# Kernel tuning notes

Measured on AMD Instinct MI355X. Metric: run time of the kernel, lower is better.

## Reference

```python
import jax, jax.numpy as jnp
from jax import lax
import numpy as np

N = 262144    # input_size (mesh nodes)
B = 16        # batch of snapshots
LAT = 16      # dims_latent
HID = 512     # intermediate fc width
NFC = 16      # num_final_channels
START = 4097  # inv_conv_start
SPLIT = NFC * START
SFC = 2       # number of space-filling curves
K, S, P = 32, 4, 16             # kernel/stride/padding (dimension==2)
OPS = (1, 1, 0)                 # output_paddings of decoder convT chain
CH = ((16, 8), (8, 4), (4, 1))  # (in,out) channels per decoder convT layer


def conv_t(x, w, b, op):
    # torch ConvTranspose1d: w [Cin,Cout,K], stride=S, padding=P, output_padding=op
    # equivalent to lhs-dilated cross-correlation with flipped, transposed kernel
    rhs = jnp.flip(w, -1).transpose(1, 0, 2)  # [Cout,Cin,K]
    y = lax.conv_general_dilated(x, rhs, (1,), [(K - 1 - P, K - 1 - P + op)],
                                 lhs_dilation=(S,),
                                 dimension_numbers=('NCH', 'OIH', 'NCH'))
    return y + b[None, :, None]


def setup_inputs() -> dict:
    key = jax.random.key(0)
    ks = jax.random.split(key, 32)
    inp = {}
    inp['x'] = jax.random.normal(ks[0], (B, LAT), jnp.float32)
    inp['fc1_w'] = jax.random.normal(ks[1], (LAT, HID), jnp.float32) * 0.1
    inp['fc1_b'] = jnp.zeros((HID,), jnp.float32)
    inp['fc2_w'] = jax.random.normal(ks[2], (HID, SFC * SPLIT), jnp.float32) * 0.02
    inp['fc2_b'] = jnp.zeros((SFC * SPLIT,), jnp.float32)
    idx = 3
    for i in range(SFC):
        for j, (ci, co) in enumerate(CH):
            inp[f'ct{i}{j}_w'] = jax.random.normal(ks[idx], (ci, co, K), jnp.float32) * 0.05
            inp[f'ct{i}{j}_b'] = jnp.zeros((co,), jnp.float32)
            idx += 1
        # NearestNeighbouring(size=N, initial_weight=1/3, num_neigh=3)
        inp[f'sp{i}_w'] = jnp.full((N, 3), 1.0 / 3.0, jnp.float32)
        inp[f'sp{i}_b'] = jnp.zeros((N,), jnp.float32)
        oi = jax.random.permutation(ks[idx], N).astype(jnp.int32)
        idx += 1
        inp[f'ord{i}'] = oi
        inp[f'minus{i}'] = jnp.concatenate([oi[:1], oi[:-1]])  # find_minus_neigh
        inp[f'plus{i}'] = jnp.concatenate([oi[1:], oi[-1:]])   # find_plus_neigh
    # final_sp: NearestNeighbouring(size=N, initial_weight=1/sfc_nums, num_neigh=sfc_nums)
    inp['fsp_w'] = jnp.full((N, SFC), 1.0 / SFC, jnp.float32)
    inp['fsp_b'] = jnp.zeros((N,), jnp.float32)
    return inp


def reference(x, fc1_w, fc1_b, fc2_w, fc2_b,
              ct00_w, ct00_b, ct01_w, ct01_b, ct02_w, ct02_b,
              ct10_w, ct10_b, ct11_w, ct11_b, ct12_w, ct12_b,
              sp0_w, sp0_b, sp1_w, sp1_b, fsp_w, fsp_b,
              ord0, minus0, plus0, ord1, minus1, plus1):
    act = jnp.tanh  # unstructured default activation
    h = act(x @ fc1_w + fc1_b)
    h = act(h @ fc2_w + fc2_b)          # [B, SFC*SPLIT]
    h = h.reshape(-1, SPLIT, SFC)
    cts = (((ct00_w, ct00_b), (ct01_w, ct01_b), (ct02_w, ct02_b)),
           ((ct10_w, ct10_b), (ct11_w, ct11_b), (ct12_w, ct12_b)))
    sps = ((sp0_w, sp0_b), (sp1_w, sp1_b))
    ords = ((minus0, ord0, plus0), (minus1, ord1, plus1))
    zs = []
    for i in range(SFC):
        b = h[..., i].reshape(-1, NFC, START)   # [B,16,4097]
        for j in range(len(CH)):
            w, bb = cts[i][j]
            b = act(conv_t(b, w, bb, OPS[j]))
        b = b.reshape(-1, N)                    # [B, N]
        m, o, p = ords[i]
        # SFC gather of (minus, self, plus) neighbors -> [B, N, 3]
        tt = jnp.stack([b[:, m], b[:, o], b[:, p]], axis=-1)
        w, bb = sps[i]
        zs.append(act(jnp.sum(tt * w, -1) + bb))
    # combine the SFC branches with the final learned weighted sum
    z = act(jnp.sum(jnp.stack(zs, -1) * fsp_w, -1) + fsp_b)  # [B, N]
    return z
```

## Files before the change

### kernel.cpp

```cpp
#include <hip/hip_runtime.h>
#include <hip/hip_bf16.h>

#define BATCH 16
#define LAT 16
#define HID 512
#define NFC 16
#define START_ 4097
#define NSFC 2
#define NMESH 262144
#define JTOT 131104
#define HB_BR_STRIDE 1048832

#define L1 16385
#define L1S 16388
#define L2 65537
#define L2S 65540
#define L3 262144

#define Y1_SZ (BATCH*8*L1S)
#define Y2_SZ (BATCH*4*L2S)
#define Y3_SZ (BATCH*L3)

__global__ __launch_bounds__(256) void k_fc1(const float* __restrict__ x,
                                             const float* __restrict__ w,
                                             const float* __restrict__ bias,
                                             float* __restrict__ h1) {
    int j = blockIdx.x * 256 + threadIdx.x;
    float acc[BATCH];
    float bv = bias[j];
#pragma unroll
    for (int b = 0; b < BATCH; ++b) acc[b] = bv;
#pragma unroll
    for (int k = 0; k < LAT; ++k) {
        float wv = w[k * HID + j];
#pragma unroll
        for (int b = 0; b < BATCH; ++b)
            acc[b] = fmaf(x[b * LAT + k], wv, acc[b]);
    }
#pragma unroll
    for (int b = 0; b < BATCH; ++b) h1[b * HID + j] = tanhf(acc[b]);
}

__global__ __launch_bounds__(256) void k_fc2(const float* __restrict__ h1,
                                             const float* __restrict__ w,
                                             const float* __restrict__ bias,
                                             float* __restrict__ hb) {
    int j = blockIdx.x * 256 + threadIdx.x;
    if (j >= JTOT) return;
    float acc[BATCH];
    float bv = bias[j];
#pragma unroll
    for (int b = 0; b < BATCH; ++b) acc[b] = bv;
#pragma unroll 8
    for (int k = 0; k < HID; ++k) {
        float wv = w[(size_t)k * JTOT + j];
#pragma unroll
        for (int b = 0; b < BATCH; ++b)
            acc[b] = fmaf(h1[b * HID + k], wv, acc[b]);
    }
    int i = j & 1;
    int s = j >> 1;
    int c = s / START_;
    int t = s - c * START_;
    float* hp = hb + (size_t)i * HB_BR_STRIDE + c * START_ + t;
#pragma unroll
    for (int b = 0; b < BATCH; ++b)
        hp[(size_t)b * (NFC * START_)] = tanhf(acc[b]);
}

template <int CIN, int COUT, int WCO, int WT>
__global__ __launch_bounds__(256) void k_conv(const float* __restrict__ xb,
                                              float* __restrict__ yb,
                                              const float* __restrict__ w0g,
                                              const float* __restrict__ w1g,
                                              const float* __restrict__ b0g,
                                              const float* __restrict__ b1g,
                                              int LIN, int LINS, int LOUT, int LOUTS,
                                              int xbs, int ybs) {
    constexpr int SROW = WT * 256 + 12;
    constexpr int SROW4 = SROW / 4;
    __shared__ __align__(16) float sx[CIN * SROW];

    const int br = blockIdx.z;
    const float* x = xb + (size_t)br * xbs;
    float* y = yb + (size_t)br * ybs;
    const float* wg = br ? w1g : w0g;
    const float* bg = br ? b1g : b0g;
    const int b = blockIdx.y;
    const int t0 = blockIdx.x * (WT * 1024);
    const int q0 = (t0 + 16) >> 2;

    for (int idx = threadIdx.x; idx < CIN * SROW; idx += 256) {
        int ci = idx / SROW;
        int sr = idx - ci * SROW;
        int s = q0 - 8 + sr;
        sx[idx] = (s >= 0 && s < LIN) ? x[(size_t)(b * CIN + ci) * LINS + s] : 0.f;
    }
    __syncthreads();

    const int wv = __builtin_amdgcn_readfirstlane((int)(threadIdx.x >> 6));
    const int lane = threadIdx.x & 63;
    constexpr int WAVES_CO = 4 / WT;
    const int wt = wv / WAVES_CO;
    const int co0 = (wv % WAVES_CO) * WCO;

    float acc[WCO][16];
#pragma unroll
    for (int cw = 0; cw < WCO; ++cw) {
        float bv = bg[co0 + cw];
#pragma unroll
        for (int e = 0; e < 16; ++e) acc[cw][e] = bv;
    }

    const int qrel4 = wt * 64 + lane;
    const float4* sx4 = (const float4*)sx;
#pragma unroll 1
    for (int ci = 0; ci < CIN; ++ci) {
        float4 A = sx4[ci * SROW4 + qrel4];
        float4 Bv = sx4[ci * SROW4 + qrel4 + 1];
        float4 Cv = sx4[ci * SROW4 + qrel4 + 2];
        float xv[12] = {A.x, A.y, A.z, A.w, Bv.x, Bv.y, Bv.z, Bv.w,
                        Cv.x, Cv.y, Cv.z, Cv.w};
        const float* wp = wg + (ci * COUT + co0) * 32;
#pragma unroll
        for (int cw = 0; cw < WCO; ++cw) {
            const float* wpc = wp + cw * 32;
#pragma unroll
            for (int d = 0; d < 8; ++d)
#pragma unroll
                for (int m = 0; m < 4; ++m)
#pragma unroll
                    for (int j = 0; j < 4; ++j)
                        acc[cw][m * 4 + j] =
                            fmaf(xv[m + 8 - d], wpc[4 * d + j], acc[cw][m * 4 + j]);
        }
    }

    const int t_lane = t0 + wt * 1024 + lane * 16;
#pragma unroll
    for (int cw = 0; cw < WCO; ++cw) {
        float* yp = y + (size_t)(b * COUT + co0 + cw) * LOUTS + t_lane;
        if (t_lane + 15 < LOUT) {
#pragma unroll
            for (int c4 = 0; c4 < 4; ++c4) {
                float4 o;
                o.x = tanhf(acc[cw][c4 * 4 + 0]);
                o.y = tanhf(acc[cw][c4 * 4 + 1]);
                o.z = tanhf(acc[cw][c4 * 4 + 2]);
                o.w = tanhf(acc[cw][c4 * 4 + 3]);
                ((float4*)yp)[c4] = o;
            }
        } else {
            for (int e = 0; e < 16; ++e)
                if (t_lane + e < LOUT) yp[e] = tanhf(acc[cw][e]);
        }
    }
}

#define C3_TT 256
#define C3_SW 71

__global__ __launch_bounds__(256) void k_conv3t(const float* __restrict__ y2g,
                                                float* __restrict__ y3t,
                                                const float* __restrict__ w0g,
                                                const float* __restrict__ w1g,
                                                const float* __restrict__ b0g,
                                                const float* __restrict__ b1g,
                                                int xbs, int ybs) {
    __shared__ float sx[BATCH * 4 * C3_SW];

    const int br = blockIdx.z;
    const float* x = y2g + (size_t)br * xbs;
    float* y = y3t + (size_t)br * ybs;
    const float* wg = br ? w1g : w0g;
    const float bv = (br ? b1g : b0g)[0];

    const int t0 = blockIdx.x * C3_TT;
    const int q0 = (t0 >> 2) + 4;
    const int s0 = q0 - 7;

    for (int idx = threadIdx.x; idx < BATCH * 4 * C3_SW; idx += 256) {
        int row = idx / C3_SW;
        int col = idx - row * C3_SW;
        int s = s0 + col;
        sx[idx] = (s >= 0 && s < L2) ? x[(size_t)row * L2S + s] : 0.f;
    }
    __syncthreads();

    const int q = threadIdx.x >> 2;
    const int bg = threadIdx.x & 3;

    float acc[4][4];
#pragma unroll
    for (int r = 0; r < 4; ++r)
#pragma unroll
        for (int bo = 0; bo < 4; ++bo) acc[r][bo] = bv;

#pragma unroll
    for (int ci = 0; ci < 4; ++ci) {
        const float* wp = wg + ci * 32;
#pragma unroll
        for (int bo = 0; bo < 4; ++bo) {
            const float* sp = sx + ((bg * 4 + bo) * 4 + ci) * C3_SW + q;
            float xv[8];
#pragma unroll
            for (int j = 0; j < 8; ++j) xv[j] = sp[j];
#pragma unroll
            for (int d = 0; d < 8; ++d)
#pragma unroll
                for (int r = 0; r < 4; ++r)
                    acc[r][bo] = fmaf(xv[7 - d], wp[4 * d + r], acc[r][bo]);
        }
    }

    const int tbase = t0 + 4 * q;
#pragma unroll
    for (int r = 0; r < 4; ++r) {
        float* yp = y + (size_t)(tbase + r) * BATCH + bg * 4;
        float4 o;
        o.x = tanhf(acc[r][0]);
        o.y = tanhf(acc[r][1]);
        o.z = tanhf(acc[r][2]);
        o.w = tanhf(acc[r][3]);
        *(float4*)yp = o;
    }
}

__global__ __launch_bounds__(256) void k_final(const float* __restrict__ y3t0,
                                               const float* __restrict__ y3t1,
                                               const int* __restrict__ ord0,
                                               const int* __restrict__ ord1,
                                               const float* __restrict__ sw0,
                                               const float* __restrict__ sb0,
                                               const float* __restrict__ sw1,
                                               const float* __restrict__ sb1,
                                               const float* __restrict__ fw,
                                               const float* __restrict__ fb,
                                               float* __restrict__ out) {
    __shared__ int i0[258], i1[258];
    __shared__ float c0[BATCH][264], c1[BATCH][264];
    const int tid = threadIdx.x;
    const int n0 = blockIdx.x * 256;
    const int n = n0 + tid;

    for (int jj = tid; jj < 258; jj += 256) {
        int nn = n0 - 1 + jj;
        nn = nn < 0 ? 0 : (nn > NMESH - 1 ? NMESH - 1 : nn);
        i0[jj] = ord0[nn];
        i1[jj] = ord1[nn];
    }
    __syncthreads();

    for (int kk = tid; kk < 258 * 4; kk += 256) {
        int jj = kk >> 2;
        int v = kk & 3;
        float4 a = *(const float4*)(y3t0 + (size_t)i0[jj] * BATCH + v * 4);
        c0[v * 4 + 0][jj] = a.x;
        c0[v * 4 + 1][jj] = a.y;
        c0[v * 4 + 2][jj] = a.z;
        c0[v * 4 + 3][jj] = a.w;
        float4 bq = *(const float4*)(y3t1 + (size_t)i1[jj] * BATCH + v * 4);
        c1[v * 4 + 0][jj] = bq.x;
        c1[v * 4 + 1][jj] = bq.y;
        c1[v * 4 + 2][jj] = bq.z;
        c1[v * 4 + 3][jj] = bq.w;
    }

    const float w00 = sw0[n * 3], w01 = sw0[n * 3 + 1], w02 = sw0[n * 3 + 2];
    const float w10 = sw1[n * 3], w11 = sw1[n * 3 + 1], w12 = sw1[n * 3 + 2];
    const float s0b = sb0[n], s1b = sb1[n];
    const float f0 = fw[n * 2], f1 = fw[n * 2 + 1], fbv = fb[n];
    __syncthreads();

#pragma unroll
    for (int b = 0; b < BATCH; ++b) {
        float z0 = tanhf(w00 * c0[b][tid] + w01 * c0[b][tid + 1] + w02 * c0[b][tid + 2] + s0b);
        float z1 = tanhf(w10 * c1[b][tid] + w11 * c1[b][tid + 1] + w12 * c1[b][tid + 2] + s1b);
        out[b * NMESH + n] = tanhf(f0 * z0 + f1 * z1 + fbv);
    }
}

extern "C" void kernel_launch(void* const* d_in, const int* in_sizes, int n_in,
                              void* d_out, int out_size, void* d_ws, size_t ws_size,
                              hipStream_t stream) {
    const float* x     = (const float*)d_in[0];
    const float* fc1_w = (const float*)d_in[1];
    const float* fc1_b = (const float*)d_in[2];
    const float* fc2_w = (const float*)d_in[3];
    const float* fc2_b = (const float*)d_in[4];
    const float* ctw[2][3] = {{(const float*)d_in[5], (const float*)d_in[7], (const float*)d_in[9]},
                              {(const float*)d_in[16], (const float*)d_in[18], (const float*)d_in[20]}};
    const float* ctb[2][3] = {{(const float*)d_in[6], (const float*)d_in[8], (const float*)d_in[10]},
                              {(const float*)d_in[17], (const float*)d_in[19], (const float*)d_in[21]}};
    const float* sp0w = (const float*)d_in[11];
    const float* sp0b = (const float*)d_in[12];
    const int*   ord0 = (const int*)d_in[13];
    const float* sp1w = (const float*)d_in[22];
    const float* sp1b = (const float*)d_in[23];
    const int*   ord1 = (const int*)d_in[24];
    const float* fspw = (const float*)d_in[27];
    const float* fspb = (const float*)d_in[28];
    float* out = (float*)d_out;
    float* ws = (float*)d_ws;

    const size_t OFF_H1 = 0;
    const size_t OFF_HB = 8192;
    const size_t OFF_Y1p = OFF_HB + 2ull * HB_BR_STRIDE;
    const size_t OFF_Y2p = OFF_Y1p + 2ull * Y1_SZ;
    const size_t OFF_Y3p = OFF_Y2p + 2ull * Y2_SZ;
    const size_t END_P = OFF_Y3p + 2ull * Y3_SZ;
    const size_t OFF_Y1s = OFF_HB + 2ull * HB_BR_STRIDE;
    const size_t OFF_Y2s = OFF_Y1s + (size_t)Y1_SZ;
    const size_t OFF_Y3s = OFF_Y2s + (size_t)Y2_SZ;

    const bool par = ws_size >= END_P * sizeof(float);

    k_fc1<<<2, 256, 0, stream>>>(x, fc1_w, fc1_b, ws + OFF_H1);
    k_fc2<<<(JTOT + 255) / 256, 256, 0, stream>>>(ws + OFF_H1, fc2_w, fc2_b, ws + OFF_HB);

    float* y3_0;
    float* y3_1;
    if (par) {
        float* hb = ws + OFF_HB;
        float* y1 = ws + OFF_Y1p;
        float* y2 = ws + OFF_Y2p;
        float* y3 = ws + OFF_Y3p;
        k_conv<16, 8, 2, 1><<<dim3(17, BATCH, 2), 256, 0, stream>>>(
            hb, y1, ctw[0][0], ctw[1][0], ctb[0][0], ctb[1][0],
            START_, START_, L1, L1S, HB_BR_STRIDE, Y1_SZ);
        k_conv<8, 4, 1, 1><<<dim3(65, BATCH, 2), 256, 0, stream>>>(
            y1, y2, ctw[0][1], ctw[1][1], ctb[0][1], ctb[1][1],
            L1, L1S, L2, L2S, Y1_SZ, Y2_SZ);
        k_conv3t<<<dim3(L3 / C3_TT, 1, 2), 256, 0, stream>>>(
            y2, y3, ctw[0][2], ctw[1][2], ctb[0][2], ctb[1][2],
            Y2_SZ, Y3_SZ);
        y3_0 = y3;
        y3_1 = y3 + Y3_SZ;
    } else {
        float* y1 = ws + OFF_Y1s;
        float* y2 = ws + OFF_Y2s;
        for (int i = 0; i < 2; ++i) {
            float* hb_i = ws + OFF_HB + (size_t)i * HB_BR_STRIDE;
            float* y3_i = ws + OFF_Y3s + (size_t)i * Y3_SZ;
            k_conv<16, 8, 2, 1><<<dim3(17, BATCH, 1), 256, 0, stream>>>(
                hb_i, y1, ctw[i][0], ctw[i][0], ctb[i][0], ctb[i][0],
                START_, START_, L1, L1S, 0, 0);
            k_conv<8, 4, 1, 1><<<dim3(65, BATCH, 1), 256, 0, stream>>>(
                y1, y2, ctw[i][1], ctw[i][1], ctb[i][1], ctb[i][1],
                L1, L1S, L2, L2S, 0, 0);
            k_conv3t<<<dim3(L3 / C3_TT, 1, 1), 256, 0, stream>>>(
                y2, y3_i, ctw[i][2], ctw[i][2], ctb[i][2], ctb[i][2],
                0, 0);
        }
        y3_0 = ws + OFF_Y3s;
        y3_1 = ws + OFF_Y3s + Y3_SZ;
    }

    k_final<<<NMESH / 256, 256, 0, stream>>>(y3_0, y3_1, ord0, ord1,
                                             sp0w, sp0b, sp1w, sp1b,
                                             fspw, fspb, out);
}
```

Baseline: 579.7 us.

## Fuse second and third transposed convolutions; use fast exp2-based tanh

Merges the conv layer 2 and conv layer 3 kernels into one. Each block computes a halo tile of the intermediate 4-channel output in shared memory, then applies the final conv straight from it, so the y2 buffer is never written to or read from global memory. All tanhf calls are also replaced with an exp2/rcp approximation to cut transcendental cost. The cost is recomputing the halo of the intermediate layer, and tanh accuracy drops, with possible inf handling issues for large inputs.

Result: no change. 588.0 us (+1.4%).

```diff
diff --git a/kernel.cpp b/kernel.cpp
--- a/kernel.cpp
+++ b/kernel.cpp
@@ -14,12 +14,15 @@
 #define L1 16385
 #define L1S 16388
 #define L2 65537
-#define L2S 65540
 #define L3 262144
 
 #define Y1_SZ (BATCH*8*L1S)
-#define Y2_SZ (BATCH*4*L2S)
 #define Y3_SZ (BATCH*L3)
+
+__device__ __forceinline__ float tanh_fast(float x) {
+    float e = __builtin_amdgcn_exp2f(x * 2.8853900817779268f);
+    return 1.0f - 2.0f * __builtin_amdgcn_rcpf(e + 1.0f);
+}
 
 __global__ __launch_bounds__(256) void k_fc1(const float* __restrict__ x,
                                              const float* __restrict__ w,
@@ -38,7 +41,7 @@
             acc[b] = fmaf(x[b * LAT + k], wv, acc[b]);
     }
 #pragma unroll
-    for (int b = 0; b < BATCH; ++b) h1[b * HID + j] = tanhf(acc[b]);
+    for (int b = 0; b < BATCH; ++b) h1[b * HID + j] = tanh_fast(acc[b]);
 }
 
 __global__ __launch_bounds__(256) void k_fc2(const float* __restrict__ h1,
@@ -65,7 +68,7 @@
     float* hp = hb + (size_t)i * HB_BR_STRIDE + c * START_ + t;
 #pragma unroll
     for (int b = 0; b < BATCH; ++b)
-        hp[(size_t)b * (NFC * START_)] = tanhf(acc[b]);
+        hp[(size_t)b * (NFC * START_)] = tanh_fast(acc[b]);
 }
 
 template <int CIN, int COUT, int WCO, int WT>
@@ -144,85 +147,134 @@
 #pragma unroll
             for (int c4 = 0; c4 < 4; ++c4) {
                 float4 o;
-                o.x = tanhf(acc[cw][c4 * 4 + 0]);
-                o.y = tanhf(acc[cw][c4 * 4 + 1]);
-                o.z = tanhf(acc[cw][c4 * 4 + 2]);
-                o.w = tanhf(acc[cw][c4 * 4 + 3]);
+                o.x = tanh_fast(acc[cw][c4 * 4 + 0]);
+                o.y = tanh_fast(acc[cw][c4 * 4 + 1]);
+                o.z = tanh_fast(acc[cw][c4 * 4 + 2]);
+                o.w = tanh_fast(acc[cw][c4 * 4 + 3]);
                 ((float4*)yp)[c4] = o;
             }
         } else {
             for (int e = 0; e < 16; ++e)
-                if (t_lane + e < LOUT) yp[e] = tanhf(acc[cw][e]);
-        }
-    }
-}
-
-#define C3_TT 256
-#define C3_SW 71
-
-__global__ __launch_bounds__(256) void k_conv3t(const float* __restrict__ y2g,
-                                                float* __restrict__ y3t,
-                                                const float* __restrict__ w0g,
-                                                const float* __restrict__ w1g,
-                                                const float* __restrict__ b0g,
-                                                const float* __restrict__ b1g,
-                                                int xbs, int ybs) {
-    __shared__ float sx[BATCH * 4 * C3_SW];
+                if (t_lane + e < LOUT) yp[e] = tanh_fast(acc[cw][e]);
+        }
+    }
+}
+
+#define F_Y1W 25
+#define F_Y2W 73
+
+__global__ __launch_bounds__(256) void k_conv23t(const float* __restrict__ y1g,
+                                                 float* __restrict__ y3t,
+                                                 const float* __restrict__ w20,
+                                                 const float* __restrict__ w21,
+                                                 const float* __restrict__ b20,
+                                                 const float* __restrict__ b21,
+                                                 const float* __restrict__ w30,
+                                                 const float* __restrict__ w31,
+                                                 const float* __restrict__ b30,
+                                                 const float* __restrict__ b31,
+                                                 int xbs, int ybs) {
+    __shared__ float s_y1[BATCH * 8 * F_Y1W];
+    __shared__ float s_y2[BATCH * 4 * F_Y2W];
 
     const int br = blockIdx.z;
-    const float* x = y2g + (size_t)br * xbs;
+    const float* x1 = y1g + (size_t)br * xbs;
     float* y = y3t + (size_t)br * ybs;
-    const float* wg = br ? w1g : w0g;
-    const float bv = (br ? b1g : b0g)[0];
-
-    const int t0 = blockIdx.x * C3_TT;
-    const int q0 = (t0 >> 2) + 4;
-    const int s0 = q0 - 7;
-
-    for (int idx = threadIdx.x; idx < BATCH * 4 * C3_SW; idx += 256) {
-        int row = idx / C3_SW;
-        int col = idx - row * C3_SW;
-        int s = s0 + col;
-        sx[idx] = (s >= 0 && s < L2) ? x[(size_t)row * L2S + s] : 0.f;
+    const float* w2 = br ? w21 : w20;
+    const float b2v_all = 0.f; (void)b2v_all;
+    const float* b2 = br ? b21 : b20;
+    const float* w3 = br ? w31 : w30;
+    const float b3v = (br ? b31 : b30)[0];
+
+    const int bx = blockIdx.x;
+    const int T0 = bx * 256;
+    const int Q1_0 = (T0 >> 4) - 4;
+    const int S2_0 = (T0 >> 2) - 4;
+
+    for (int idx = threadIdx.x; idx < BATCH * 8 * F_Y1W; idx += 256) {
+        int row = idx / F_Y1W;
+        int col = idx - row * F_Y1W;
+        int q1 = Q1_0 + col;
+        s_y1[idx] = (q1 >= 0 && q1 < L1) ? x1[(size_t)row * L1S + q1] : 0.f;
     }
     __syncthreads();
 
-    const int q = threadIdx.x >> 2;
-    const int bg = threadIdx.x & 3;
-
-    float acc[4][4];
-#pragma unroll
-    for (int r = 0; r < 4; ++r)
-#pragma unroll
-        for (int bo = 0; bo < 4; ++bo) acc[r][bo] = bv;
-
-#pragma unroll
-    for (int ci = 0; ci < 4; ++ci) {
-        const float* wp = wg + ci * 32;
-#pragma unroll
-        for (int bo = 0; bo < 4; ++bo) {
-            const float* sp = sx + ((bg * 4 + bo) * 4 + ci) * C3_SW + q;
-            float xv[8];
-#pragma unroll
-            for (int j = 0; j < 8; ++j) xv[j] = sp[j];
-#pragma unroll
-            for (int d = 0; d < 8; ++d)
-#pragma unroll
-                for (int r = 0; r < 4; ++r)
-                    acc[r][bo] = fmaf(xv[7 - d], wp[4 * d + r], acc[r][bo]);
-        }
-    }
-
-    const int tbase = t0 + 4 * q;
-#pragma unroll
-    for (int r = 0; r < 4; ++r) {
-        float* yp = y + (size_t)(tbase + r) * BATCH + bg * 4;
-        float4 o;
-        o.x = tanhf(acc[r][0]);
-        o.y = tanhf(acc[r][1]);
-        o.z = tanhf(acc[r][2]);
-        o.w = tanhf(acc[r][3]);
-        *(float4*)yp = o;
+    {
+        const int wv = __builtin_amdgcn_readfirstlane((int)(threadIdx.x >> 6));
+        const int lane = threadIdx.x & 63;
+        const int b = lane & 15;
+        const int gg = lane >> 4;
+        const float b2v = b2[wv];
+#pragma unroll
+        for (int j5 = 0; j5 < 5; ++j5) {
+            int g = gg + 4 * j5;
+            if (g < 18) {
+                float acc[4];
+#pragma unroll
+                for (int r = 0; r < 4; ++r) acc[r] = b2v;
+#pragma unroll
+                for (int ci = 0; ci < 8; ++ci) {
+                    const float* sp = s_y1 + (b * 8 + ci) * F_Y1W + g;
+                    float xv[8];
+#pragma unroll
+                    for (int jj = 0; jj < 8; ++jj) xv[jj] = sp[jj];
+                    const float* wpc = w2 + (ci * 4 + wv) * 32;
+#pragma unroll
+                    for (int d = 0; d < 8; ++d)
+#pragma unroll
+                        for (int r = 0; r < 4; ++r)
+                            acc[r] = fmaf(xv[7 - d], wpc[4 * d + r], acc[r]);
+                }
+                int s2b = S2_0 + 4 * g;
+                float* dst = s_y2 + (b * 4 + wv) * F_Y2W + 4 * g;
+#pragma unroll
+                for (int r = 0; r < 4; ++r) {
+                    int s2 = s2b + r;
+                    dst[r] = (s2 >= 0 && s2 < L2) ? tanh_fast(acc[r]) : 0.f;
+                }
+            }
+        }
+    }
+    __syncthreads();
+
+    {
+        const int q = threadIdx.x >> 2;
+        const int bg = threadIdx.x & 3;
+
+        float acc[4][4];
+#pragma unroll
+        for (int r = 0; r < 4; ++r)
+#pragma unroll
+            for (int bo = 0; bo < 4; ++bo) acc[r][bo] = b3v;
+
+#pragma unroll
+        for (int ci = 0; ci < 4; ++ci) {
+            const float* wp = w3 + ci * 32;
+#pragma unroll
+            for (int bo = 0; bo < 4; ++bo) {
+                const float* sp = s_y2 + ((bg * 4 + bo) * 4 + ci) * F_Y2W + q + 1;
+                float xv[8];
+#pragma unroll
+                for (int j = 0; j < 8; ++j) xv[j] = sp[j];
+#pragma unroll
+                for (int d = 0; d < 8; ++d)
+#pragma unroll
+                    for (int r = 0; r < 4; ++r)
+                        acc[r][bo] = fmaf(xv[7 - d], wp[4 * d + r], acc[r][bo]);
+            }
+        }
+
+        const int tbase = T0 + 4 * q;
+#pragma unroll
+        for (int r = 0; r < 4; ++r) {
+            float* yp = y + (size_t)(tbase + r) * BATCH + bg * 4;
+            float4 o;
+            o.x = tanh_fast(acc[r][0]);
+            o.y = tanh_fast(acc[r][1]);
+            o.z = tanh_fast(acc[r][2]);
+            o.w = tanh_fast(acc[r][3]);
+            *(float4*)yp = o;
+        }
     }
 }
 
@@ -274,9 +326,9 @@
 
 #pragma unroll
     for (int b = 0; b < BATCH; ++b) {
-        float z0 = tanhf(w00 * c0[b][tid] + w01 * c0[b][tid + 1] + w02 * c0[b][tid + 2] + s0b);
-        float z1 = tanhf(w10 * c1[b][tid] + w11 * c1[b][tid + 1] + w12 * c1[b][tid + 2] + s1b);
-        out[b * NMESH + n] = tanhf(f0 * z0 + f1 * z1 + fbv);
+        float z0 = tanh_fast(w00 * c0[b][tid] + w01 * c0[b][tid + 1] + w02 * c0[b][tid + 2] + s0b);
+        float z1 = tanh_fast(w10 * c1[b][tid] + w11 * c1[b][tid + 1] + w12 * c1[b][tid + 2] + s1b);
+        out[b * NMESH + n] = tanh_fast(f0 * z0 + f1 * z1 + fbv);
     }
 }
 
@@ -306,12 +358,10 @@
     const size_t OFF_H1 = 0;
     const size_t OFF_HB = 8192;
     const size_t OFF_Y1p = OFF_HB + 2ull * HB_BR_STRIDE;
-    const size_t OFF_Y2p = OFF_Y1p + 2ull * Y1_SZ;
-    const size_t OFF_Y3p = OFF_Y2p + 2ull * Y2_SZ;
+    const size_t OFF_Y3p = OFF_Y1p + 2ull * Y1_SZ;
     const size_t END_P = OFF_Y3p + 2ull * Y3_SZ;
     const size_t OFF_Y1s = OFF_HB + 2ull * HB_BR_STRIDE;
-    const size_t OFF_Y2s = OFF_Y1s + (size_t)Y1_SZ;
-    const size_t OFF_Y3s = OFF_Y2s + (size_t)Y2_SZ;
+    const size_t OFF_Y3s = OFF_Y1s + (size_t)Y1_SZ;
 
     const bool par = ws_size >= END_P * sizeof(float);
 
@@ -323,33 +373,27 @@
     if (par) {
         float* hb = ws + OFF_HB;
         float* y1 = ws + OFF_Y1p;
-        float* y2 = ws + OFF_Y2p;
         float* y3 = ws + OFF_Y3p;
         k_conv<16, 8, 2, 1><<<dim3(17, BATCH, 2), 256, 0, stream>>>(
             hb, y1, ctw[0][0], ctw[1][0], ctb[0][0], ctb[1][0],
             START_, START_, L1, L1S, HB_BR_STRIDE, Y1_SZ);
-        k_conv<8, 4, 1, 1><<<dim3(65, BATCH, 2), 256, 0, stream>>>(
-            y1, y2, ctw[0][1], ctw[1][1], ctb[0][1], ctb[1][1],
-            L1, L1S, L2, L2S, Y1_SZ, Y2_SZ);
-        k_conv3t<<<dim3(L3 / C3_TT, 1, 2), 256, 0, stream>>>(
-            y2, y3, ctw[0][2], ctw[1][2], ctb[0][2], ctb[1][2],
-            Y2_SZ, Y3_SZ);
+        k_conv23t<<<dim3(L3 / 256, 1, 2), 256, 0, stream>>>(
+            y1, y3, ctw[0][1], ctw[1][1], ctb[0][1], ctb[1][1],
+            ctw[0][2], ctw[1][2], ctb[0][2], ctb[1][2],
+            Y1_SZ, Y3_SZ);
         y3_0 = y3;
         y3_1 = y3 + Y3_SZ;
     } else {
         float* y1 = ws + OFF_Y1s;
-        float* y2 = ws + OFF_Y2s;
         for (int i = 0; i < 2; ++i) {
             float* hb_i = ws + OFF_HB + (size_t)i * HB_BR_STRIDE;
             float* y3_i = ws + OFF_Y3s + (size_t)i * Y3_SZ;
             k_conv<16, 8, 2, 1><<<dim3(17, BATCH, 1), 256, 0, stream>>>(
                 hb_i, y1, ctw[i][0], ctw[i][0], ctb[i][0], ctb[i][0],
                 START_, START_, L1, L1S, 0, 0);
-            k_conv<8, 4, 1, 1><<<dim3(65, BATCH, 1), 256, 0, stream>>>(
-                y1, y2, ctw[i][1], ctw[i][1], ctb[i][1], ctb[i][1],
-                L1, L1S, L2, L2S, 0, 0);
-            k_conv3t<<<dim3(L3 / C3_TT, 1, 1), 256, 0, stream>>>(
-                y2, y3_i, ctw[i][2], ctw[i][2], ctb[i][2], ctb[i][2],
+            k_conv23t<<<dim3(L3 / 256, 1, 1), 256, 0, stream>>>(
+                y1, y3_i, ctw[i][1], ctw[i][1], ctb[i][1], ctb[i][1],
+                ctw[i][2], ctw[i][2], ctb[i][2], ctb[i][2],
                 0, 0);
         }
         y3_0 = ws + OFF_Y3s;
```
